# Kernel tuning notes

Hardware: AMD Instinct MI355X
Metric: run time of the kernel (lower is better)

The kernel has to match this reference:

```python
import jax, jax.numpy as jnp
import numpy as np

HEADS = 9
QK = 64   # qk_embed_dim = in_dim // num_heads = 576 // 9
VD = 64   # v_dim
KVS = 2   # kv_stride


def conv3x3(x, w):
    return jax.lax.conv_general_dilated(
        x, w, (1, 1), 'SAME', dimension_numbers=('NCHW', 'OIHW', 'NCHW'))


def deform_conv3x3(x, offset, w):
    """Deformable conv v1, 3x3, stride 1, pad 1, 1 deformable group.
    x: (n,C,H,W); offset: (n,18,H,W) channel layout [dy0,dx0,dy1,dx1,...]; w: (O,C,3,3).
    """
    n, C, H, W = x.shape
    ky, kx = jnp.meshgrid(jnp.arange(3, dtype=x.dtype), jnp.arange(3, dtype=x.dtype), indexing='ij')
    ky = ky.reshape(9)
    kx = kx.reshape(9)
    off = offset.reshape(n, 9, 2, H, W)
    ys = jnp.arange(H, dtype=x.dtype)
    xs = jnp.arange(W, dtype=x.dtype)
    # sampling positions: out_pos - pad + kernel_pos + learned offset -> (n,9,H,W)
    py = ys[None, None, :, None] - 1.0 + ky[None, :, None, None] + off[:, :, 0]
    px = xs[None, None, None, :] - 1.0 + kx[None, :, None, None] + off[:, :, 1]
    y0 = jnp.floor(py)
    x0 = jnp.floor(px)
    dy = py - y0
    dx = px - x0
    xf = x.reshape(n, C, H * W)

    def gather(yi, xi):
        valid = ((yi >= 0) & (yi < H) & (xi >= 0) & (xi < W)).astype(x.dtype)
        yc = jnp.clip(yi, 0, H - 1).astype(jnp.int32)
        xc = jnp.clip(xi, 0, W - 1).astype(jnp.int32)
        idx = (yc * W + xc).reshape(n, 1, 9 * H * W)
        v = jnp.take_along_axis(xf, idx, axis=2).reshape(n, C, 9, H, W)
        return v * valid[:, None]

    samp = (((1 - dy) * (1 - dx))[:, None] * gather(y0, x0)
            + ((1 - dy) * dx)[:, None] * gather(y0, x0 + 1)
            + (dy * (1 - dx))[:, None] * gather(y0 + 1, x0)
            + (dy * dx)[:, None] * gather(y0 + 1, x0 + 1))  # (n,C,9,H,W)
    return jnp.einsum('ock,nckhw->nohw', w.reshape(w.shape[0], C, 9), samp)


def setup_inputs() -> dict:
    key = jax.random.key(0)
    ks = jax.random.split(key, 10)
    n, C, H, W = 2, 576, 64, 64
    s1 = 1.0 / np.sqrt(C)
    s9 = 1.0 / np.sqrt(C * 9)
    return {
        'x': jax.random.normal(ks[0], (n, C, H, W), jnp.float32),
        'key_w': jax.random.normal(ks[1], (C, C), jnp.float32) * s1,
        'offset_w': jax.random.normal(ks[2], (18, C, 3, 3), jnp.float32) * 0.01,
        'dconv_w': jax.random.normal(ks[3], (C, C, 3, 3), jnp.float32) * s9,
        'value_w': jax.random.normal(ks[4], (C, C), jnp.float32) * s1,
        'proj_w': jax.random.normal(ks[5], (C, C), jnp.float32) * s1,
        'proj_b': jax.random.normal(ks[6], (C,), jnp.float32) * 0.01,
        'appr_bias': jax.random.normal(ks[7], (C,), jnp.float32) * s1,
        'appr_bias_q': jax.random.normal(ks[8], (C,), jnp.float32) * s1,
        'gamma': jax.random.normal(ks[9], (1,), jnp.float32) * 0.1,
    }


def reference(x, key_w, offset_w, dconv_w, value_w, proj_w, proj_b, appr_bias, appr_bias_q, gamma):
    n, C, H, W = x.shape
    x_q = x                              # q_stride == 1
    x_kv = x[:, :, ::KVS, ::KVS]         # AvgPool2d(kernel=1, stride=2)
    hk, wk = x_kv.shape[2], x_kv.shape[3]
    # key content term (appr_bias . key): per-kv scalar per head
    proj_key = jnp.einsum('oc,nchw->nohw', key_w, x_kv).reshape(n, HEADS, QK, hk * wk)
    b = jnp.einsum('he,nhek->nhk', appr_bias.reshape(HEADS, QK), proj_key)
    # query relative-position term via deformable conv: per-query scalar per head
    offset = conv3x3(x_q, offset_w)
    pq = deform_conv3x3(x_q, offset, dconv_w).reshape(n, HEADS, QK, H * W)
    a = jnp.einsum('he,nheq->nhq', appr_bias_q.reshape(HEADS, QK), pq)
    # energy (n, heads, HW, hk*wk); attention_type[0] is False so energy is a+b broadcast
    energy = a[..., :, None] + b[..., None, :]
    attn = jax.nn.softmax(energy, axis=-1)
    v = jnp.einsum('oc,nchw->nohw', value_w, x_kv).reshape(n, HEADS, VD, hk * wk)
    out = jnp.einsum('nhqk,nhdk->nhdq', attn, v).reshape(n, HEADS * VD, H, W)
    out = jnp.einsum('oc,nchw->nohw', proj_w, out) + proj_b[None, :, None, None]
    return gamma * out + x
```

## Files before the change

### kernel.cpp

```cpp
#include <hip/hip_runtime.h>


#define CCH 576
#define NH 9
#define HW 4096
#define KHW 1024
#define W 64
#define CHN 16
#define CPC 36

#define WS_XKV   0
#define WS_BPART 1179648
#define WS_P     (1179648 + 294912)
#define WS_WX    (1179648 + 294912 + 18432)
#define WS_OV    (1179648 + 294912 + 18432 + 10368)

__global__ void k_bpart(const float* __restrict__ x, const float* __restrict__ key_w,
                        const float* __restrict__ appr_bias, float* __restrict__ bpart,
                        float* __restrict__ xkv) {
    int k  = blockIdx.x * 256 + threadIdx.x;
    int n  = blockIdx.y;
    int ch = blockIdx.z;
    int c0 = ch * CPC;

    __shared__ float ab[CCH];
    __shared__ float kbs[NH][CPC];
    for (int i = threadIdx.x; i < CCH; i += 256) ab[i] = appr_bias[i];
    __syncthreads();
    for (int t = threadIdx.x; t < NH * CPC; t += 256) {
        int h = t / CPC, cl = t % CPC;
        float s = 0.f;
        #pragma unroll 8
        for (int e = 0; e < 64; ++e)
            s += ab[h * 64 + e] * key_w[(size_t)(h * 64 + e) * CCH + c0 + cl];
        kbs[h][cl] = s;
    }
    __syncthreads();

    int ky = k >> 5, kx = k & 31;
    const float* xb = x + (size_t)n * CCH * HW + (size_t)c0 * HW + (size_t)(ky * 2) * W + kx * 2;
    float acc[NH];
    #pragma unroll
    for (int h = 0; h < NH; ++h) acc[h] = 0.f;
    for (int cl = 0; cl < CPC; ++cl) {
        float xv = xb[(size_t)cl * HW];
        xkv[((size_t)n * CCH + c0 + cl) * KHW + k] = xv;
        #pragma unroll
        for (int h = 0; h < NH; ++h) acc[h] += kbs[h][cl] * xv;
    }
    #pragma unroll
    for (int h = 0; h < NH; ++h)
        bpart[(((size_t)n * CHN + ch) * NH + h) * KHW + k] = acc[h];
}

__global__ void k_softmax(const float* __restrict__ bpart, float* __restrict__ p) {
    int nh = blockIdx.x;
    int n = nh / NH, h = nh % NH;
    int tid = threadIdx.x;
    int wave = tid >> 6, lane = tid & 63;
    float s[4];
    #pragma unroll
    for (int j = 0; j < 4; ++j) {
        int k = tid + j * 256;
        float v = 0.f;
        #pragma unroll
        for (int ch = 0; ch < CHN; ++ch)
            v += bpart[(((size_t)n * CHN + ch) * NH + h) * KHW + k];
        s[j] = v;
    }
    float m = fmaxf(fmaxf(s[0], s[1]), fmaxf(s[2], s[3]));
    #pragma unroll
    for (int off = 32; off >= 1; off >>= 1)
        m = fmaxf(m, __shfl_xor(m, off, 64));
    __shared__ float redm[4];
    if (lane == 0) redm[wave] = m;
    __syncthreads();
    m = fmaxf(fmaxf(redm[0], redm[1]), fmaxf(redm[2], redm[3]));
    float e[4], lsum = 0.f;
    #pragma unroll
    for (int j = 0; j < 4; ++j) { e[j] = __expf(s[j] - m); lsum += e[j]; }
    #pragma unroll
    for (int off = 32; off >= 1; off >>= 1)
        lsum += __shfl_xor(lsum, off, 64);
    __shared__ float reds[4];
    if (lane == 0) reds[wave] = lsum;
    __syncthreads();
    float inv = 1.f / (reds[0] + reds[1] + reds[2] + reds[3]);
    #pragma unroll
    for (int j = 0; j < 4; ++j)
        p[(size_t)nh * KHW + tid + j * 256] = e[j] * inv;
}

__global__ void k_wx(const float* __restrict__ xkv, const float* __restrict__ p,
                     float* __restrict__ wx) {
    int n = blockIdx.y;
    int tid = threadIdx.x;
    int wv = tid >> 6, ln = tid & 63;
    __shared__ float ps[NH * KHW];
    const float4* p4 = (const float4*)(p + (size_t)n * NH * KHW);
    float4* ps4 = (float4*)ps;
    for (int i = tid; i < NH * KHW / 4; i += 256) ps4[i] = p4[i];
    __syncthreads();

    int c = blockIdx.x * 4 + wv;
    const float4* xr = (const float4*)(xkv + ((size_t)n * CCH + c) * KHW);
    float acc[NH];
    #pragma unroll
    for (int h = 0; h < NH; ++h) acc[h] = 0.f;
    #pragma unroll
    for (int j = 0; j < 4; ++j) {
        float4 xv = xr[ln + 64 * j];
        #pragma unroll
        for (int h = 0; h < NH; ++h) {
            float4 pv = ((const float4*)(ps + h * KHW))[ln + 64 * j];
            acc[h] += pv.x * xv.x + pv.y * xv.y + pv.z * xv.z + pv.w * xv.w;
        }
    }
    #pragma unroll
    for (int h = 0; h < NH; ++h) {
        float v = acc[h];
        #pragma unroll
        for (int off = 32; off >= 1; off >>= 1) v += __shfl_xor(v, off, 64);
        if (ln == 0) wx[((size_t)n * NH + h) * CCH + c] = v;
    }
}

__global__ void k_ov(const float* __restrict__ value_w, const float* __restrict__ wx,
                     float* __restrict__ ov) {
    int g = blockIdx.x * 4 + (threadIdx.x >> 6);
    int lane = threadIdx.x & 63;
    int n = g / CCH, o = g % CCH;
    int h = o >> 6;
    const float* vw  = value_w + (size_t)o * CCH;
    const float* wxr = wx + ((size_t)n * NH + h) * CCH;
    float acc = 0.f;
    #pragma unroll
    for (int j = 0; j < 9; ++j)
        acc += vw[lane + 64 * j] * wxr[lane + 64 * j];
    #pragma unroll
    for (int off = 32; off >= 1; off >>= 1)
        acc += __shfl_xor(acc, off, 64);
    if (lane == 0) ov[n * CCH + o] = acc;
}

__global__ void k_pofinal(const float* __restrict__ proj_w, const float* __restrict__ proj_b,
                          const float* __restrict__ ov, const float* __restrict__ x,
                          const float* __restrict__ gamma, float* __restrict__ out) {
    int b = blockIdx.x;
    int n = b / CCH, o = b % CCH;
    int t = threadIdx.x;
    int wv = t >> 6, ln = t & 63;
    __shared__ float pr[4];

    const float* pw  = proj_w + (size_t)o * CCH;
    const float* ovr = ov + n * CCH;
    float acc = pw[t] * ovr[t] + pw[t + 256] * ovr[t + 256];
    if (t < 64) acc += pw[t + 512] * ovr[t + 512];
    #pragma unroll
    for (int off = 32; off >= 1; off >>= 1)
        acc += __shfl_xor(acc, off, 64);
    if (ln == 0) pr[wv] = acc;
    __syncthreads();
    float base = gamma[0] * ((pr[0] + pr[1] + pr[2] + pr[3]) + proj_b[o]);

    const float4* x4 = (const float4*)(x + ((size_t)n * CCH + o) * HW);
    float4* o4 = (float4*)(out + ((size_t)n * CCH + o) * HW);
    #pragma unroll
    for (int j = 0; j < 4; ++j) {
        int idx = t + 256 * j;
        float4 v = x4[idx];
        v.x += base; v.y += base; v.z += base; v.w += base;
        o4[idx] = v;
    }
}

extern "C" void kernel_launch(void* const* d_in, const int* in_sizes, int n_in,
                              void* d_out, int out_size, void* d_ws, size_t ws_size,
                              hipStream_t stream) {
    const float* x         = (const float*)d_in[0];
    const float* key_w     = (const float*)d_in[1];
    const float* value_w   = (const float*)d_in[4];
    const float* proj_w    = (const float*)d_in[5];
    const float* proj_b    = (const float*)d_in[6];
    const float* appr_bias = (const float*)d_in[7];
    const float* gamma     = (const float*)d_in[9];
    float* out = (float*)d_out;

    float* ws    = (float*)d_ws;
    float* xkv   = ws + WS_XKV;
    float* bpart = ws + WS_BPART;
    float* p     = ws + WS_P;
    float* wx    = ws + WS_WX;
    float* ov    = ws + WS_OV;

    k_bpart  <<<dim3(4, 2, CHN), 256, 0, stream>>>(x, key_w, appr_bias, bpart, xkv);
    k_softmax<<<18, 256, 0, stream>>>(bpart, p);
    k_wx     <<<dim3(144, 2), 256, 0, stream>>>(xkv, p, wx);
    k_ov     <<<288, 256, 0, stream>>>(value_w, wx, ov);
    k_pofinal<<<1152, 256, 0, stream>>>(proj_w, proj_b, ov, x, gamma, out);
}
```

Before: 41.82 us.

## Drop xkv staging buffer, read strided x directly, split projection from final add

Removes the intermediate xkv buffer written by k_bpart; k_wx now gathers the stride-2 kv samples straight from x. Softmax is vectorised to float4 loads and stores. The fused projection+residual kernel is split into a small per-channel projection kernel plus a grid-stride elementwise add. The aim is to cut global write/read traffic for xkv and to make the final add a bandwidth-friendly flat stream, at the cost of one extra launch and strided uncoalesced reads of x in k_wx.

```diff
diff --git a/kernel.cpp b/kernel.cpp
--- a/kernel.cpp
+++ b/kernel.cpp
@@ -9,15 +9,14 @@
 #define CHN 16
 #define CPC 36
 
-#define WS_XKV   0
-#define WS_BPART 1179648
-#define WS_P     (1179648 + 294912)
-#define WS_WX    (1179648 + 294912 + 18432)
-#define WS_OV    (1179648 + 294912 + 18432 + 10368)
+#define WS_BPART 0
+#define WS_P     294912
+#define WS_WX    (294912 + 18432)
+#define WS_OV    (294912 + 18432 + 10368)
+#define WS_PO    (294912 + 18432 + 10368 + 1152)
 
 __global__ void k_bpart(const float* __restrict__ x, const float* __restrict__ key_w,
-                        const float* __restrict__ appr_bias, float* __restrict__ bpart,
-                        float* __restrict__ xkv) {
+                        const float* __restrict__ appr_bias, float* __restrict__ bpart) {
     int k  = blockIdx.x * 256 + threadIdx.x;
     int n  = blockIdx.y;
     int ch = blockIdx.z;
@@ -29,10 +28,11 @@
     __syncthreads();
     for (int t = threadIdx.x; t < NH * CPC; t += 256) {
         int h = t / CPC, cl = t % CPC;
+        const float* kwr = key_w + (size_t)(h * 64) * CCH + c0 + cl;
         float s = 0.f;
-        #pragma unroll 8
+        #pragma unroll
         for (int e = 0; e < 64; ++e)
-            s += ab[h * 64 + e] * key_w[(size_t)(h * 64 + e) * CCH + c0 + cl];
+            s += ab[h * 64 + e] * kwr[(size_t)e * CCH];
         kbs[h][cl] = s;
     }
     __syncthreads();
@@ -42,9 +42,9 @@
     float acc[NH];
     #pragma unroll
     for (int h = 0; h < NH; ++h) acc[h] = 0.f;
+    #pragma unroll 12
     for (int cl = 0; cl < CPC; ++cl) {
         float xv = xb[(size_t)cl * HW];
-        xkv[((size_t)n * CCH + c0 + cl) * KHW + k] = xv;
         #pragma unroll
         for (int h = 0; h < NH; ++h) acc[h] += kbs[h][cl] * xv;
     }
@@ -58,17 +58,15 @@
     int n = nh / NH, h = nh % NH;
     int tid = threadIdx.x;
     int wave = tid >> 6, lane = tid & 63;
-    float s[4];
-    #pragma unroll
-    for (int j = 0; j < 4; ++j) {
-        int k = tid + j * 256;
-        float v = 0.f;
-        #pragma unroll
-        for (int ch = 0; ch < CHN; ++ch)
-            v += bpart[(((size_t)n * CHN + ch) * NH + h) * KHW + k];
-        s[j] = v;
-    }
-    float m = fmaxf(fmaxf(s[0], s[1]), fmaxf(s[2], s[3]));
+    const float4* bp4 = (const float4*)bpart;
+
+    float4 s = make_float4(0.f, 0.f, 0.f, 0.f);
+    #pragma unroll
+    for (int ch = 0; ch < CHN; ++ch) {
+        float4 b = bp4[(((size_t)n * CHN + ch) * NH + h) * (KHW / 4) + tid];
+        s.x += b.x; s.y += b.y; s.z += b.z; s.w += b.w;
+    }
+    float m = fmaxf(fmaxf(s.x, s.y), fmaxf(s.z, s.w));
     #pragma unroll
     for (int off = 32; off >= 1; off >>= 1)
         m = fmaxf(m, __shfl_xor(m, off, 64));
@@ -76,9 +74,11 @@
     if (lane == 0) redm[wave] = m;
     __syncthreads();
     m = fmaxf(fmaxf(redm[0], redm[1]), fmaxf(redm[2], redm[3]));
-    float e[4], lsum = 0.f;
-    #pragma unroll
-    for (int j = 0; j < 4; ++j) { e[j] = __expf(s[j] - m); lsum += e[j]; }
+
+    float4 e;
+    e.x = __expf(s.x - m); e.y = __expf(s.y - m);
+    e.z = __expf(s.z - m); e.w = __expf(s.w - m);
+    float lsum = e.x + e.y + e.z + e.w;
     #pragma unroll
     for (int off = 32; off >= 1; off >>= 1)
         lsum += __shfl_xor(lsum, off, 64);
@@ -86,12 +86,11 @@
     if (lane == 0) reds[wave] = lsum;
     __syncthreads();
     float inv = 1.f / (reds[0] + reds[1] + reds[2] + reds[3]);
-    #pragma unroll
-    for (int j = 0; j < 4; ++j)
-        p[(size_t)nh * KHW + tid + j * 256] = e[j] * inv;
-}
-
-__global__ void k_wx(const float* __restrict__ xkv, const float* __restrict__ p,
+    e.x *= inv; e.y *= inv; e.z *= inv; e.w *= inv;
+    ((float4*)p)[(size_t)nh * (KHW / 4) + tid] = e;
+}
+
+__global__ void k_wx(const float* __restrict__ x, const float* __restrict__ p,
                      float* __restrict__ wx) {
     int n = blockIdx.y;
     int tid = threadIdx.x;
@@ -103,18 +102,17 @@
     __syncthreads();
 
     int c = blockIdx.x * 4 + wv;
-    const float4* xr = (const float4*)(xkv + ((size_t)n * CCH + c) * KHW);
+    const float* xb = x + ((size_t)n * CCH + c) * HW;
     float acc[NH];
     #pragma unroll
     for (int h = 0; h < NH; ++h) acc[h] = 0.f;
     #pragma unroll
-    for (int j = 0; j < 4; ++j) {
-        float4 xv = xr[ln + 64 * j];
-        #pragma unroll
-        for (int h = 0; h < NH; ++h) {
-            float4 pv = ((const float4*)(ps + h * KHW))[ln + 64 * j];
-            acc[h] += pv.x * xv.x + pv.y * xv.y + pv.z * xv.z + pv.w * xv.w;
-        }
+    for (int j = 0; j < 16; ++j) {
+        int k = ln + 64 * j;
+        int ky = k >> 5, kx = k & 31;
+        float xv = xb[(size_t)(ky * 2) * W + kx * 2];
+        #pragma unroll
+        for (int h = 0; h < NH; ++h) acc[h] += ps[h * KHW + k] * xv;
     }
     #pragma unroll
     for (int h = 0; h < NH; ++h) {
@@ -143,34 +141,36 @@
     if (lane == 0) ov[n * CCH + o] = acc;
 }
 
-__global__ void k_pofinal(const float* __restrict__ proj_w, const float* __restrict__ proj_b,
-                          const float* __restrict__ ov, const float* __restrict__ x,
-                          const float* __restrict__ gamma, float* __restrict__ out) {
-    int b = blockIdx.x;
-    int n = b / CCH, o = b % CCH;
-    int t = threadIdx.x;
-    int wv = t >> 6, ln = t & 63;
-    __shared__ float pr[4];
-
+__global__ void k_po(const float* __restrict__ proj_w, const float* __restrict__ proj_b,
+                     const float* __restrict__ ov, float* __restrict__ po) {
+    int g = blockIdx.x * 4 + (threadIdx.x >> 6);
+    int lane = threadIdx.x & 63;
+    int n = g / CCH, o = g % CCH;
     const float* pw  = proj_w + (size_t)o * CCH;
     const float* ovr = ov + n * CCH;
-    float acc = pw[t] * ovr[t] + pw[t + 256] * ovr[t + 256];
-    if (t < 64) acc += pw[t + 512] * ovr[t + 512];
+    float acc = 0.f;
+    #pragma unroll
+    for (int j = 0; j < 9; ++j)
+        acc += pw[lane + 64 * j] * ovr[lane + 64 * j];
     #pragma unroll
     for (int off = 32; off >= 1; off >>= 1)
         acc += __shfl_xor(acc, off, 64);
-    if (ln == 0) pr[wv] = acc;
-    __syncthreads();
-    float base = gamma[0] * ((pr[0] + pr[1] + pr[2] + pr[3]) + proj_b[o]);
-
-    const float4* x4 = (const float4*)(x + ((size_t)n * CCH + o) * HW);
-    float4* o4 = (float4*)(out + ((size_t)n * CCH + o) * HW);
-    #pragma unroll
-    for (int j = 0; j < 4; ++j) {
-        int idx = t + 256 * j;
-        float4 v = x4[idx];
+    if (lane == 0) po[n * CCH + o] = acc + proj_b[o];
+}
+
+__global__ void k_final(const float* __restrict__ x, const float* __restrict__ po,
+                        const float* __restrict__ gamma, float* __restrict__ out) {
+    const size_t total4 = (size_t)2 * CCH * HW / 4;
+    float g = gamma[0];
+    const float4* x4 = (const float4*)x;
+    float4* o4 = (float4*)out;
+    for (size_t i = (size_t)blockIdx.x * blockDim.x + threadIdx.x; i < total4;
+         i += (size_t)gridDim.x * blockDim.x) {
+        int no = (int)(i >> 10);
+        float base = g * po[no];
+        float4 v = x4[i];
         v.x += base; v.y += base; v.z += base; v.w += base;
-        o4[idx] = v;
+        o4[i] = v;
     }
 }
 
@@ -187,15 +187,16 @@
     float* out = (float*)d_out;
 
     float* ws    = (float*)d_ws;
-    float* xkv   = ws + WS_XKV;
     float* bpart = ws + WS_BPART;
     float* p     = ws + WS_P;
     float* wx    = ws + WS_WX;
     float* ov    = ws + WS_OV;
-
-    k_bpart  <<<dim3(4, 2, CHN), 256, 0, stream>>>(x, key_w, appr_bias, bpart, xkv);
+    float* po    = ws + WS_PO;
+
+    k_bpart  <<<dim3(4, 2, CHN), 256, 0, stream>>>(x, key_w, appr_bias, bpart);
     k_softmax<<<18, 256, 0, stream>>>(bpart, p);
-    k_wx     <<<dim3(144, 2), 256, 0, stream>>>(xkv, p, wx);
+    k_wx     <<<dim3(144, 2), 256, 0, stream>>>(x, p, wx);
     k_ov     <<<288, 256, 0, stream>>>(value_w, wx, ov);
-    k_pofinal<<<1152, 256, 0, stream>>>(proj_w, proj_b, ov, x, gamma, out);
-}
+    k_po     <<<288, 256, 0, stream>>>(proj_w, proj_b, ov, po);
+    k_final  <<<2048, 256, 0, stream>>>(x, po, gamma, out);
+}
```

Measured after the change: 48.18 us. +15.2%, slower.
